# Kernel optimization log

Hardware: AMD Instinct MI355X
Metric: run time of the kernel (lower is better)

Reference implementation:

```python
import jax, jax.numpy as jnp
import numpy as np

B, C, H, W = 4, 320, 32, 32
HEADS = 8
LTXT, DCROSS = 77, 768
HW = H * W


def _ln(x, w, b, eps=1e-5):
    mu = x.mean(-1, keepdims=True)
    var = jnp.var(x, axis=-1, keepdims=True)
    return (x - mu) * jax.lax.rsqrt(var + eps) * w + b


def _gn(x, w, b, groups=32, eps=1e-6):
    Bx, Cx, Hx, Wx = x.shape
    xg = x.reshape(Bx, groups, -1)
    mu = xg.mean(-1, keepdims=True)
    var = jnp.var(xg, axis=-1, keepdims=True)
    xn = ((xg - mu) * jax.lax.rsqrt(var + eps)).reshape(Bx, Cx, Hx, Wx)
    return xn * w[None, :, None, None] + b[None, :, None, None]


def _attn(q, k, v, bias=None):
    Bq, S, Cd = q.shape
    dh = Cd // HEADS
    qh = q.reshape(Bq, S, HEADS, dh)
    kh = k.reshape(Bq, -1, HEADS, dh)
    vh = v.reshape(Bq, -1, HEADS, dh)
    s = jnp.einsum('bqhd,bkhd->bhqk', qh, kh) * (1.0 / np.sqrt(dh))
    if bias is not None:
        s = s + bias  # additive 0/1 otsu mask, exactly as the torch code passes it
    p = jax.nn.softmax(s, axis=-1)
    o = jnp.einsum('bhqk,bkhd->bqhd', p, vh).reshape(Bq, S, Cd)
    return o, p


def _block(x, ctx, prm, bias=None):
    # BasicTransformerBlock: self-attn -> cross-attn (returns probs) -> GEGLU FF
    (ln1w, ln1b, qkv, ow, ob, ln2w, ln2b, q2, kv2, o2w, o2b,
     ln3w, ln3b, ff1w, ff1b, ff2w, ff2b) = prm
    h = _ln(x, ln1w, ln1b)
    q, k, v = jnp.split(h @ qkv, 3, axis=-1)
    o, _ = _attn(q, k, v)
    x = x + o @ ow + ob
    h = _ln(x, ln2w, ln2b)
    k2, v2 = jnp.split(ctx @ kv2, 2, axis=-1)
    o2, p2 = _attn(h @ q2, k2, v2, bias)
    x = x + o2 @ o2w + o2b
    h = _ln(x, ln3w, ln3b)
    a, g = jnp.split(h @ ff1w + ff1b, 2, axis=-1)
    x = x + (a * jax.nn.gelu(g)) @ ff2w + ff2b
    return x, p2


def _otsu(m):
    # vectorized version of the 10-threshold otsu loop (m: [B/2, N])
    mn = m.min(-1, keepdims=True)
    mx = m.max(-1, keepdims=True)
    x = (m - mn) / (mx - mn)
    n = x.shape[-1]
    ts = jnp.arange(10, dtype=x.dtype) * 0.1  # thresholds t*0.1
    low = x[:, None, :] < ts[None, :, None]   # [B/2, 10, N]
    cnt_low = low.sum(-1).astype(x.dtype)
    cnt_high = n - cnt_low
    sum_low = jnp.where(low, x[:, None, :], 0.0).sum(-1)
    sum_high = x.sum(-1, keepdims=True) - sum_low
    mu_low = jnp.where(cnt_low > 0, sum_low / jnp.maximum(cnt_low, 1.0), jnp.nan)
    mu_high = jnp.where(cnt_high > 0, sum_high / jnp.maximum(cnt_high, 1.0), jnp.nan)
    g = (cnt_low / n) * (cnt_high / n) * (mu_low - mu_high) ** 2
    g = jnp.where(jnp.isnan(g), -jnp.inf, g)  # torch: nan > max_g is False -> skipped
    best = jnp.argmax(g, axis=-1)             # first max == torch strict-> ties keep earliest
    gmax = jnp.take_along_axis(g, best[:, None], axis=-1)[:, 0]
    thr = jnp.where(gmax > 0, best.astype(x.dtype) * 0.1, 0.0)[:, None]
    return jnp.where(x < thr, 0.0, jnp.where(x > thr, 1.0, x))


def _fwd(gn_w, gn_b, pin_w, pin_b,
         b_ln1w, b_ln1b, b_qkv, b_ow, b_ob, b_ln2w, b_ln2b, b_q2, b_kv2, b_o2w, b_o2b,
         b_ln3w, b_ln3b, b_ff1w, b_ff1b, b_ff2w, b_ff2b,
         i_ln1w, i_ln1b, i_qkv, i_ow, i_ob, i_ln2w, i_ln2b, i_q2, i_kv2, i_o2w, i_o2b,
         i_ln3w, i_ln3b, i_ff1w, i_ff1b, i_ff2w, i_ff2b,
         pout_w, pout_b, hidden_states, encoder_hidden_states,
         ph_b, ph_t, eot_b, eot_t):
    residual = hidden_states
    h = _gn(hidden_states, gn_w, gn_b)
    h = h.transpose(0, 2, 3, 1).reshape(B, HW, C)
    h = h @ pin_w + pin_b  # use_linear_projection path
    blk = (b_ln1w, b_ln1b, b_qkv, b_ow, b_ob, b_ln2w, b_ln2b, b_q2, b_kv2, b_o2w, b_o2b,
           b_ln3w, b_ln3b, b_ff1w, b_ff1b, b_ff2w, b_ff2b)
    iblk = (i_ln1w, i_ln1b, i_qkv, i_ow, i_ob, i_ln2w, i_ln2b, i_q2, i_kv2, i_o2w, i_o2b,
            i_ln3w, i_ln3b, i_ff1w, i_ff1b, i_ff2w, i_ff2b)
    h, probs = _block(h, encoder_hidden_states, blk)   # probs [B, heads, HW, 77]
    ap = probs.mean(1)[B // 2:]                        # head-avg attn_probs, cond half
    attn = ap.transpose(0, 2, 1)                       # [B/2, 77, HW]
    attn_ph = attn[ph_b, ph_t]                         # [B/2, HW]
    attn_eot = jax.lax.stop_gradient(attn[eot_b, eot_t])
    loss_reg = jnp.mean((attn_ph / attn_ph.max(-1, keepdims=True)
                         - attn_eot / attn_eot.max(-1, keepdims=True)) ** 2)
    mask = _otsu(jax.lax.stop_gradient(attn_ph))       # [B/2, HW]
    bias = mask[:, None, None, :]                      # broadcast over heads and queries
    hs, img = h[:B // 2], h[B // 2:]
    hs, _ = _block(hs, img, iblk, bias)                # image_cross_attention
    h = jnp.concatenate([hs, img], axis=0)
    h = h @ pout_w + pout_b
    sample = h.reshape(B, H, W, C).transpose(0, 3, 1, 2) + residual
    return sample, loss_reg


def setup_inputs():
    key = jax.random.key(0)
    ki = iter(jax.random.split(key, 80))
    f32 = jnp.float32

    def rn(shape, s=0.02):
        return jax.random.normal(next(ki), shape, f32) * s

    def blk(p, cross):
        return {p + 'ln1w': jnp.ones((C,), f32), p + 'ln1b': jnp.zeros((C,), f32),
                p + 'qkv': rn((C, 3 * C)), p + 'ow': rn((C, C)), p + 'ob': jnp.zeros((C,), f32),
                p + 'ln2w': jnp.ones((C,), f32), p + 'ln2b': jnp.zeros((C,), f32),
                p + 'q2': rn((C, C)), p + 'kv2': rn((cross, 2 * C)),
                p + 'o2w': rn((C, C)), p + 'o2b': jnp.zeros((C,), f32),
                p + 'ln3w': jnp.ones((C,), f32), p + 'ln3b': jnp.zeros((C,), f32),
                p + 'ff1w': rn((C, 8 * C)), p + 'ff1b': jnp.zeros((8 * C,), f32),
                p + 'ff2w': rn((4 * C, C)), p + 'ff2b': jnp.zeros((C,), f32)}

    inp = {'gn_w': jnp.ones((C,), f32), 'gn_b': jnp.zeros((C,), f32),
           'pin_w': rn((C, C)), 'pin_b': jnp.zeros((C,), f32)}
    inp.update(blk('b_', DCROSS))
    inp.update(blk('i_', C))
    inp['pout_w'] = rn((C, C))
    inp['pout_b'] = jnp.zeros((C,), f32)
    inp['hidden_states'] = jax.random.normal(next(ki), (B, C, H, W), f32)
    inp['encoder_hidden_states'] = jax.random.normal(next(ki), (B, LTXT, DCROSS), f32)
    inp['ph_b'] = jnp.arange(B // 2)
    inp['ph_t'] = jax.random.randint(next(ki), (B // 2,), 0, LTXT)
    inp['eot_b'] = jnp.arange(B // 2)
    inp['eot_t'] = jax.random.randint(next(ki), (B // 2,), 0, LTXT)
    return inp


def reference(gn_w, gn_b, pin_w, pin_b,
              b_ln1w, b_ln1b, b_qkv, b_ow, b_ob, b_ln2w, b_ln2b, b_q2, b_kv2, b_o2w, b_o2b,
              b_ln3w, b_ln3b, b_ff1w, b_ff1b, b_ff2w, b_ff2b,
              i_ln1w, i_ln1b, i_qkv, i_ow, i_ob, i_ln2w, i_ln2b, i_q2, i_kv2, i_o2w, i_o2b,
              i_ln3w, i_ln3b, i_ff1w, i_ff1b, i_ff2w, i_ff2b,
              pout_w, pout_b, hidden_states, encoder_hidden_states,
              ph_b, ph_t, eot_b, eot_t):
    return _fwd(gn_w, gn_b, pin_w, pin_b,
                b_ln1w, b_ln1b, b_qkv, b_ow, b_ob, b_ln2w, b_ln2b, b_q2, b_kv2, b_o2w, b_o2b,
                b_ln3w, b_ln3b, b_ff1w, b_ff1b, b_ff2w, b_ff2b,
                i_ln1w, i_ln1b, i_qkv, i_ow, i_ob, i_ln2w, i_ln2b, i_q2, i_kv2, i_o2w, i_o2b,
                i_ln3w, i_ln3b, i_ff1w, i_ff1b, i_ff2w, i_ff2b,
                pout_w, pout_b, hidden_states, encoder_hidden_states,
                ph_b, ph_t, eot_b, eot_t)
```

## Files before the change

### kernel.cpp

```cpp
#include <hip/hip_runtime.h>
#include <hip/hip_bf16.h>
#include <math.h>

#define NH 8
#define DH 40
#define CCH 320
#define SCALE 0.15811388300841897f

typedef __attribute__((ext_vector_type(8))) short short8;
typedef __attribute__((ext_vector_type(4))) float float4v;

static __device__ __forceinline__ unsigned short f2bf(float x) {
  __hip_bfloat16 t = __float2bfloat16(x);
  return *reinterpret_cast<unsigned short*>(&t);
}

static __device__ __forceinline__ void gload16(const void* g, void* l) {
  __builtin_amdgcn_global_load_lds((__attribute__((address_space(1))) void*)g,
                                   (__attribute__((address_space(3))) void*)l, 16, 0, 0);
}

__global__ __launch_bounds__(256) void gn_kernel(const float* __restrict__ x,
                                                 const float* __restrict__ w,
                                                 const float* __restrict__ b,
                                                 unsigned short* __restrict__ out) {
  int batch = blockIdx.x >> 5;
  int g = blockIdx.x & 31;
  const int CPG = 10;
  const float* xp = x + ((size_t)batch * CCH + g * CPG) * 1024;
  float s = 0.f, ss = 0.f;
  for (int i = threadIdx.x; i < CPG * 1024; i += 256) { float v = xp[i]; s += v; ss += v * v; }
  __shared__ float r1[256], r2[256];
  r1[threadIdx.x] = s; r2[threadIdx.x] = ss; __syncthreads();
  for (int off = 128; off > 0; off >>= 1) {
    if (threadIdx.x < off) { r1[threadIdx.x] += r1[threadIdx.x + off]; r2[threadIdx.x] += r2[threadIdx.x + off]; }
    __syncthreads();
  }
  float mu = r1[0] * (1.f / 10240.f);
  float var = r2[0] * (1.f / 10240.f) - mu * mu;
  float inv = rsqrtf(var + 1e-6f);
  for (int i = threadIdx.x; i < CPG * 1024; i += 256) {
    int ci = i >> 10; int hw = i & 1023; int c = g * CPG + ci;
    float v = (xp[i] - mu) * inv * w[c] + b[c];
    out[((size_t)batch * 1024 + hw) * CCH + c] = f2bf(v);
  }
}

struct WTab {
  const float* src[16];
  unsigned short* dst[16];
  int Kd[16];
  int Nd[16];
  int perm[16];
  int tstart[17];
  float* lz;
};
__global__ __launch_bounds__(256) void wconv_kernel(WTab t) {
  __shared__ float tile[32][33];
  if (blockIdx.x == 0 && threadIdx.x == 0) *t.lz = 0.f;
  int gid = blockIdx.x;
  int w = 0;
  while (w < 15 && gid >= t.tstart[w + 1]) w++;
  int local = gid - t.tstart[w];
  int K = t.Kd[w], N = t.Nd[w];
  int ntx = (N + 31) >> 5;
  int bx = local % ntx, by = local / ntx;
  int nb = bx * 32, kb = by * 32;
  const float* src = t.src[w];
  unsigned short* dst = t.dst[w];
  int doperm = t.perm[w];
  int half = N >> 1;
  int tx = threadIdx.x & 31, ty = threadIdx.x >> 5;
  for (int i = ty; i < 32; i += 8) {
    int k = kb + i, n = nb + tx;
    tile[i][tx] = (k < K && n < N) ? src[(size_t)k * N + n] : 0.f;
  }
  __syncthreads();
  for (int i = ty; i < 32; i += 8) {
    int n = nb + i, k = kb + tx;
    if (n < N && k < K) {
      int nd = n;
      if (doperm) {
        if (n < half) nd = (n >> 5) * 64 + (n & 31);
        else { int c = n - half; nd = (c >> 5) * 64 + 32 + (c & 31); }
      }
      dst[(size_t)nd * K + k] = f2bf(tile[tx][i]);
    }
  }
}

__global__ __launch_bounds__(256) void lngemm64_kernel(const float* __restrict__ A,
                                                       const float* __restrict__ lnw,
                                                       const float* __restrict__ lnb,
                                                       const unsigned short* __restrict__ Bt,
                                                       const float* __restrict__ bias,
                                                       unsigned short* __restrict__ outp,
                                                       int M, int N, int gl) {
  __shared__ unsigned short As[64][328];
  __shared__ unsigned short Bsd[2][64][32];
  __shared__ float Wf[320], Bf[320];
  __shared__ float Mu[64], Iv[64];
  const int K = 320;
  int tid = threadIdx.x;
  int lane = tid & 63;
  int wv = tid >> 6;
  int quad = lane >> 4;
  int col = lane & 15;
  int m0 = blockIdx.y * 64;
  int n0 = blockIdx.x * 64;
  const unsigned short* bp0 = Bt + (size_t)(n0 + (tid >> 2)) * K + (tid & 3) * 8;
  gload16(bp0, ((char*)Bsd[0]) + wv * 1024);
  for (int i = tid; i < 320; i += 256) { Wf[i] = lnw[i]; Bf[i] = lnb[i]; }
  int l32 = tid & 31;
  int rsub = tid >> 5;
  for (int it = 0; it < 8; it++) {
    int r = it * 8 + rsub;
    const float* ap = A + (size_t)(m0 + r) * K;
    float s = 0.f, ss = 0.f;
#pragma unroll
    for (int j = 0; j < 10; j++) { float v = ap[l32 + j * 32]; s += v; ss += v * v; }
#pragma unroll
    for (int o = 16; o > 0; o >>= 1) { s += __shfl_xor(s, o); ss += __shfl_xor(ss, o); }
    if (l32 == 0) {
      float mu = s * (1.f / 320.f);
      Mu[r] = mu;
      Iv[r] = rsqrtf(ss * (1.f / 320.f) - mu * mu + 1e-5f);
    }
  }
  __syncthreads();
#pragma unroll 4
  for (int i = 0; i < 20; i++) {
    int cc = i * 256 + tid;
    int r = cc / 80, c4 = cc - r * 80;
    int c = c4 * 4;
    float4 v = *(const float4*)(A + (size_t)(m0 + r) * K + c);
    float mu = Mu[r], iv = Iv[r];
    ushort4 o;
    o.x = f2bf((v.x - mu) * iv * Wf[c] + Bf[c]);
    o.y = f2bf((v.y - mu) * iv * Wf[c + 1] + Bf[c + 1]);
    o.z = f2bf((v.z - mu) * iv * Wf[c + 2] + Bf[c + 2]);
    o.w = f2bf((v.w - mu) * iv * Wf[c + 3] + Bf[c + 3]);
    *(ushort4*)&As[r][c] = o;
  }
  __syncthreads();
  float4v acc[4];
  float4v zero = {0.f, 0.f, 0.f, 0.f};
#pragma unroll
  for (int j = 0; j < 4; j++) acc[j] = zero;
  for (int t = 0; t < 10; t++) {
    if (t < 9) gload16(bp0 + (t + 1) * 32, ((char*)Bsd[(t + 1) & 1]) + wv * 1024);
    int k0 = t * 32;
    short8 af = *(short8*)&As[wv * 16 + col][k0 + quad * 8];
#pragma unroll
    for (int j = 0; j < 4; j++) {
      short8 bfr = *(short8*)&Bsd[t & 1][j * 16 + col][quad * 8];
      acc[j] = __builtin_amdgcn_mfma_f32_16x16x32_bf16(af, bfr, acc[j], 0, 0, 0);
    }
    __syncthreads();
  }
  if (gl) {
    int half = N >> 1;
#pragma unroll
    for (int jb = 0; jb < 2; jb++) {
      int nout = (n0 >> 1) + jb * 16 + col;
      float ba = bias[nout];
      float bg = bias[half + nout];
#pragma unroll
      for (int r = 0; r < 4; r++) {
        int m = m0 + wv * 16 + quad * 4 + r;
        float a = acc[jb][r] + ba;
        float g = acc[jb + 2][r] + bg;
        float t2 = tanhf(0.7978845608028654f * (g + 0.044715f * g * g * g));
        outp[(size_t)m * half + nout] = f2bf(a * (0.5f * g * (1.f + t2)));
      }
    }
    return;
  }
#pragma unroll
  for (int j = 0; j < 4; j++) {
    int n = n0 + j * 16 + col;
#pragma unroll
    for (int r = 0; r < 4; r++) {
      int m = m0 + wv * 16 + quad * 4 + r;
      outp[(size_t)m * N + n] = f2bf(acc[j][r]);
    }
  }
}

__global__ __launch_bounds__(256) void mergegemm64_kernel(const float* __restrict__ Opart,
                                                          const float* __restrict__ mpart,
                                                          const float* __restrict__ lpart,
                                                          const unsigned short* __restrict__ Bt,
                                                          const float* __restrict__ bias,
                                                          float* __restrict__ h, int M) {
  __shared__ unsigned short As[64][328];
  __shared__ unsigned short Bsd[2][64][32];
  const int K = 320;
  int tid = threadIdx.x;
  int lane = tid & 63;
  int wv = tid >> 6;
  int quad = lane >> 4;
  int col = lane & 15;
  int m0 = blockIdx.y * 64;
  int n0 = blockIdx.x * 64;
  const unsigned short* bp0 = Bt + (size_t)(n0 + (tid >> 2)) * K + (tid & 3) * 8;
  gload16(bp0, ((char*)Bsd[0]) + wv * 1024);
#pragma unroll
  for (int i = 0; i < 10; i++) {
    int cc = i * 256 + tid;
    int r = cc / 40, c8 = cc - r * 40;
    int c = c8 * 8;
    int hh = c / 40;
    int d = c - hh * 40;
    int m = m0 + r, b = m >> 10, q = m & 1023;
    size_t ri = ((size_t)(b * NH + hh) * 1024 + q) * 4;
    float ma = mpart[ri], mb = mpart[ri + 1], mc = mpart[ri + 2], md = mpart[ri + 3];
    float Mx = fmaxf(fmaxf(ma, mb), fmaxf(mc, md));
    float w0 = __expf(ma - Mx), w1 = __expf(mb - Mx), w2 = __expf(mc - Mx), w3 = __expf(md - Mx);
    float L = lpart[ri] * w0 + lpart[ri + 1] * w1 + lpart[ri + 2] * w2 + lpart[ri + 3] * w3;
    float inv = 1.f / L;
    w0 *= inv; w1 *= inv; w2 *= inv; w3 *= inv;
    const float* p0 = Opart + (ri + 0) * DH + d;
    const float* p1 = Opart + (ri + 1) * DH + d;
    const float* p2 = Opart + (ri + 2) * DH + d;
    const float* p3 = Opart + (ri + 3) * DH + d;
    float4 a0 = *(const float4*)p0, a1 = *(const float4*)p1, a2 = *(const float4*)p2, a3 = *(const float4*)p3;
    float4 b0 = *(const float4*)(p0 + 4), b1 = *(const float4*)(p1 + 4), b2 = *(const float4*)(p2 + 4), b3 = *(const float4*)(p3 + 4);
    ushort4 u0, u1;
    u0.x = f2bf(a0.x * w0 + a1.x * w1 + a2.x * w2 + a3.x * w3);
    u0.y = f2bf(a0.y * w0 + a1.y * w1 + a2.y * w2 + a3.y * w3);
    u0.z = f2bf(a0.z * w0 + a1.z * w1 + a2.z * w2 + a3.z * w3);
    u0.w = f2bf(a0.w * w0 + a1.w * w1 + a2.w * w2 + a3.w * w3);
    u1.x = f2bf(b0.x * w0 + b1.x * w1 + b2.x * w2 + b3.x * w3);
    u1.y = f2bf(b0.y * w0 + b1.y * w1 + b2.y * w2 + b3.y * w3);
    u1.z = f2bf(b0.z * w0 + b1.z * w1 + b2.z * w2 + b3.z * w3);
    u1.w = f2bf(b0.w * w0 + b1.w * w1 + b2.w * w2 + b3.w * w3);
    *(ushort4*)&As[r][c] = u0;
    *(ushort4*)&As[r][c + 4] = u1;
  }
  __syncthreads();
  float4v acc[4];
  float4v zero = {0.f, 0.f, 0.f, 0.f};
#pragma unroll
  for (int j = 0; j < 4; j++) acc[j] = zero;
  for (int t = 0; t < 10; t++) {
    if (t < 9) gload16(bp0 + (t + 1) * 32, ((char*)Bsd[(t + 1) & 1]) + wv * 1024);
    int k0 = t * 32;
    short8 af = *(short8*)&As[wv * 16 + col][k0 + quad * 8];
#pragma unroll
    for (int j = 0; j < 4; j++) {
      short8 bfr = *(short8*)&Bsd[t & 1][j * 16 + col][quad * 8];
      acc[j] = __builtin_amdgcn_mfma_f32_16x16x32_bf16(af, bfr, acc[j], 0, 0, 0);
    }
    __syncthreads();
  }
#pragma unroll
  for (int j = 0; j < 4; j++) {
    int n = n0 + j * 16 + col;
    float bv = bias[n];
#pragma unroll
    for (int r = 0; r < 4; r++) {
      int m = m0 + wv * 16 + quad * 4 + r;
      size_t oi = (size_t)m * 320 + n;
      h[oi] = acc[j][r] + bv + h[oi];
    }
  }
}

__global__ __launch_bounds__(256) void mgemm64_kernel(const void* __restrict__ Ap,
                                                      const unsigned short* __restrict__ Bt,
                                                      const float* __restrict__ bias,
                                                      const float* __restrict__ res,
                                                      void* __restrict__ outp,
                                                      int M, int N, int K, int a32, int omode) {
  __shared__ unsigned short As[64][160];
  __shared__ unsigned short Bs[64][160];
  int tid = threadIdx.x;
  int lane = tid & 63;
  int wv = tid >> 6;
  int quad = lane >> 4;
  int col = lane & 15;
  int m0 = blockIdx.y * 64;
  int n0 = blockIdx.x * 64;
  float4v acc[4];
  float4v zero = {0.f, 0.f, 0.f, 0.f};
#pragma unroll
  for (int j = 0; j < 4; j++) acc[j] = zero;
  short8 vzero = {0, 0, 0, 0, 0, 0, 0, 0};
  int kfast = (!a32) && ((K % 160) == 0);
  int off[5];
#pragma unroll
  for (int i = 0; i < 5; i++) { int c = i * 256 + tid; int row = c / 20; off[i] = row * K + (c - row * 20) * 8; }
  int wb = (tid & 192) * 16;
  const unsigned short* Ab = (const unsigned short*)Ap + (size_t)m0 * K;
  const unsigned short* Bb = Bt + (size_t)n0 * K;
  for (int k0 = 0; k0 < K; k0 += 160) {
    if (kfast) {
#pragma unroll
      for (int i = 0; i < 5; i++) {
        gload16(Ab + off[i] + k0, ((char*)As) + wb + i * 4096);
        gload16(Bb + off[i] + k0, ((char*)Bs) + wb + i * 4096);
      }
    } else {
#pragma unroll
      for (int i = 0; i < 5; i++) {
        int u = tid + i * 256;
        int row = u / 20, seg = u - row * 20;
        int k = k0 + seg * 8;
        int m = m0 + row;
        short8 av = vzero;
        if (m < M && k < K) {
          if (a32) {
            const float* Af = (const float*)Ap;
            float4 f0 = *(const float4*)(Af + (size_t)m * K + k);
            float4 f1 = *(const float4*)(Af + (size_t)m * K + k + 4);
            av[0] = (short)f2bf(f0.x); av[1] = (short)f2bf(f0.y);
            av[2] = (short)f2bf(f0.z); av[3] = (short)f2bf(f0.w);
            av[4] = (short)f2bf(f1.x); av[5] = (short)f2bf(f1.y);
            av[6] = (short)f2bf(f1.z); av[7] = (short)f2bf(f1.w);
          } else {
            av = *(const short8*)((const unsigned short*)Ap + (size_t)m * K + k);
          }
        }
        *(short8*)&As[row][seg * 8] = av;
        int n = n0 + row;
        short8 bv = vzero;
        if (n < N && k < K) bv = *(const short8*)(Bt + (size_t)n * K + k);
        *(short8*)&Bs[row][seg * 8] = bv;
      }
    }
    __syncthreads();
#pragma unroll
    for (int kk = 0; kk < 5; kk++) {
      int kq2 = kk * 32 + quad * 8;
      short8 af = *(short8*)&As[wv * 16 + col][kq2];
#pragma unroll
      for (int j = 0; j < 4; j++) {
        short8 bfr = *(short8*)&Bs[j * 16 + col][kq2];
        acc[j] = __builtin_amdgcn_mfma_f32_16x16x32_bf16(af, bfr, acc[j], 0, 0, 0);
      }
    }
    __syncthreads();
  }
#pragma unroll
  for (int j = 0; j < 4; j++) {
    int n = n0 + j * 16 + col;
    if (n >= N) continue;
    float bv = bias ? bias[n] : 0.f;
#pragma unroll
    for (int r = 0; r < 4; r++) {
      int m = m0 + wv * 16 + quad * 4 + r;
      if (m < M) {
        float v = acc[j][r] + bv;
        if (omode == 2) {
          int bq = m >> 10, hw = m & 1023;
          size_t oi = ((size_t)bq * N + n) * 1024 + hw;
          ((float*)outp)[oi] = v + res[oi];
        } else {
          if (res) v += res[(size_t)m * N + n];
          if (omode == 1) ((unsigned short*)outp)[(size_t)m * N + n] = f2bf(v);
          else ((float*)outp)[(size_t)m * N + n] = v;
        }
      }
    }
  }
}

#define VSTR 72
__global__ __launch_bounds__(256) void mfattns_kernel(const unsigned short* __restrict__ qp, int qstr,
                                                      const unsigned short* __restrict__ kp, int kstr,
                                                      const unsigned short* __restrict__ vp, int vstr,
                                                      const float* __restrict__ bias,
                                                      float* __restrict__ Opart,
                                                      float* __restrict__ mpart,
                                                      float* __restrict__ lpart) {
  __shared__ unsigned short Ks[64 * 56];
  __shared__ unsigned short Vt[48 * VSTR];
  __shared__ unsigned short Ps[4][16 * 72];
  int tid = threadIdx.x;
  int lane = tid & 63;
  int wv = tid >> 6;
  int quad = lane >> 4;
  int col = lane & 15;
  int bid = blockIdx.x;
  int split = bid & 3;
  int qt = (bid >> 2) & 15;
  int h = (bid >> 6) & 7;
  int b = bid >> 9;

  short8 zero8 = {0, 0, 0, 0, 0, 0, 0, 0};
  int qrow = qt * 64 + wv * 16 + col;
  const unsigned short* qbase = qp + (size_t)(b * 1024 + qrow) * qstr + h * DH;
  short8 qf0 = *(const short8*)(qbase + quad * 8);
  short8 qf1 = (quad == 0) ? *(const short8*)(qbase + 32) : zero8;

  float4v Oacc[3];
  float4v fzero = {0.f, 0.f, 0.f, 0.f};
  Oacc[0] = fzero; Oacc[1] = fzero; Oacc[2] = fzero;
  float mr[4] = {-3.4e38f, -3.4e38f, -3.4e38f, -3.4e38f};
  float lr[4] = {0.f, 0.f, 0.f, 0.f};

  for (int kt = split * 4; kt < split * 4 + 4; kt++) {
    int kb = kt * 64;
    __syncthreads();
    for (int u = tid; u < 384; u += 256) {
      int key = u / 6, s = u - key * 6;
      short8 kv8 = zero8;
      if (s < 5) kv8 = *(const short8*)(kp + (size_t)(b * 1024 + kb + key) * kstr + h * DH + s * 8);
      *(short8*)&Ks[key * 56 + s * 8] = kv8;
    }
    for (int u = tid; u < 384; u += 256) {
      int s = u >> 6, key = u & 63;
      short8 vv8 = zero8;
      if (s < 5) vv8 = *(const short8*)(vp + (size_t)(b * 1024 + kb + key) * vstr + h * DH + s * 8);
#pragma unroll
      for (int j = 0; j < 8; j++) Vt[(s * 8 + j) * VSTR + key] = (unsigned short)vv8[j];
    }
    __syncthreads();

    float4v sf[4];
#pragma unroll
    for (int jb = 0; jb < 4; jb++) {
      const unsigned short* krow = &Ks[(jb * 16 + col) * 56];
      short8 bk0 = *(const short8*)(krow + quad * 8);
      short8 bk1 = (quad == 0) ? *(const short8*)(krow + 32) : zero8;
      float4v s = fzero;
      s = __builtin_amdgcn_mfma_f32_16x16x32_bf16(qf0, bk0, s, 0, 0, 0);
      s = __builtin_amdgcn_mfma_f32_16x16x32_bf16(qf1, bk1, s, 0, 0, 0);
      float bv = bias ? bias[b * 1024 + kb + jb * 16 + col] : 0.f;
#pragma unroll
      for (int r = 0; r < 4; r++) s[r] = s[r] * SCALE + bv;
      sf[jb] = s;
    }
    float tmax[4];
#pragma unroll
    for (int r = 0; r < 4; r++) {
      float t = fmaxf(fmaxf(sf[0][r], sf[1][r]), fmaxf(sf[2][r], sf[3][r]));
#pragma unroll
      for (int o = 1; o < 16; o <<= 1) t = fmaxf(t, __shfl_xor(t, o));
      tmax[r] = t;
    }
    float al[4];
#pragma unroll
    for (int r = 0; r < 4; r++) {
      float mnew = fmaxf(mr[r], tmax[r]);
      al[r] = __expf(mr[r] - mnew);
      mr[r] = mnew;
      lr[r] *= al[r];
    }
#pragma unroll
    for (int nb = 0; nb < 3; nb++)
#pragma unroll
      for (int r = 0; r < 4; r++) Oacc[nb][r] *= al[r];
    float rs[4] = {0.f, 0.f, 0.f, 0.f};
#pragma unroll
    for (int jb = 0; jb < 4; jb++) {
#pragma unroll
      for (int r = 0; r < 4; r++) {
        float p = __expf(sf[jb][r] - mr[r]);
        rs[r] += p;
        Ps[wv][(quad * 4 + r) * 72 + jb * 16 + col] = f2bf(p);
      }
    }
#pragma unroll
    for (int r = 0; r < 4; r++) {
      float t = rs[r];
#pragma unroll
      for (int o = 1; o < 16; o <<= 1) t += __shfl_xor(t, o);
      lr[r] += t;
    }
#pragma unroll
    for (int kc = 0; kc < 2; kc++) {
      int koff = kc * 32 + quad * 8;
      short8 pa = *(const short8*)&Ps[wv][col * 72 + koff];
#pragma unroll
      for (int nb = 0; nb < 3; nb++) {
        short8 vb = *(const short8*)&Vt[(nb * 16 + col) * VSTR + koff];
        Oacc[nb] = __builtin_amdgcn_mfma_f32_16x16x32_bf16(pa, vb, Oacc[nb], 0, 0, 0);
      }
    }
  }
#pragma unroll
  for (int r = 0; r < 4; r++) {
    int qo = qt * 64 + wv * 16 + quad * 4 + r;
    size_t rowidx = (size_t)(b * NH + h) * 1024 + qo;
    float* orow = Opart + (rowidx * 4 + split) * DH;
#pragma unroll
    for (int nb = 0; nb < 3; nb++) {
      int d = nb * 16 + col;
      if (d < DH) orow[d] = Oacc[nb][r];
    }
    if (col == 0) {
      mpart[rowidx * 4 + split] = mr[r];
      lpart[rowidx * 4 + split] = lr[r];
    }
  }
}

#define CVSTR 104
__global__ __launch_bounds__(256) void cattnm_kernel(const unsigned short* __restrict__ qp,
                                                     const unsigned short* __restrict__ kvp,
                                                     unsigned short* __restrict__ op,
                                                     float* __restrict__ probs) {
  __shared__ unsigned short Ks[80 * 56];
  __shared__ unsigned short Vt[48 * CVSTR];
  __shared__ unsigned short Ps[4][16 * 104];
  int tid = threadIdx.x;
  int lane = tid & 63;
  int wv = tid >> 6;
  int quad = lane >> 4;
  int col = lane & 15;
  int bid = blockIdx.x;
  int qt = bid & 15;
  int h = (bid >> 4) & 7;
  int b = bid >> 7;

  short8 zero8 = {0, 0, 0, 0, 0, 0, 0, 0};
  for (int u = tid; u < 480; u += 256) {
    int key = u / 6, s = u - key * 6;
    short8 v8 = zero8;
    if (s < 5 && key < 77) v8 = *(const short8*)(kvp + (size_t)(b * 77 + key) * 640 + h * DH + s * 8);
    *(short8*)&Ks[key * 56 + s * 8] = v8;
  }
  for (int u = tid; u < 576; u += 256) {
    int s = u / 96, key = u - s * 96;
    short8 v8 = zero8;
    if (s < 5 && key < 77) v8 = *(const short8*)(kvp + (size_t)(b * 77 + key) * 640 + 320 + h * DH + s * 8);
#pragma unroll
    for (int j = 0; j < 8; j++) Vt[(s * 8 + j) * CVSTR + key] = (unsigned short)v8[j];
  }
  int qrow = qt * 64 + wv * 16 + col;
  const unsigned short* qbase = qp + (size_t)(b * 1024 + qrow) * CCH + h * DH;
  short8 qf0 = *(const short8*)(qbase + quad * 8);
  short8 qf1 = (quad == 0) ? *(const short8*)(qbase + 32) : zero8;
  __syncthreads();

  float4v fzero = {0.f, 0.f, 0.f, 0.f};
  float4v sf[5];
#pragma unroll
  for (int jb = 0; jb < 5; jb++) {
    const unsigned short* krow = &Ks[(jb * 16 + col) * 56];
    short8 bk0 = *(const short8*)(krow + quad * 8);
    short8 bk1 = (quad == 0) ? *(const short8*)(krow + 32) : zero8;
    float4v s = fzero;
    s = __builtin_amdgcn_mfma_f32_16x16x32_bf16(qf0, bk0, s, 0, 0, 0);
    s = __builtin_amdgcn_mfma_f32_16x16x32_bf16(qf1, bk1, s, 0, 0, 0);
    int key = jb * 16 + col;
    float msk = (key < 77) ? 0.f : -3.4e38f;
#pragma unroll
    for (int r = 0; r < 4; r++) s[r] = s[r] * SCALE + msk;
    sf[jb] = s;
  }
  float inv[4];
#pragma unroll
  for (int r = 0; r < 4; r++) {
    float t = sf[0][r];
#pragma unroll
    for (int jb = 1; jb < 5; jb++) t = fmaxf(t, sf[jb][r]);
#pragma unroll
    for (int o = 1; o < 16; o <<= 1) t = fmaxf(t, __shfl_xor(t, o));
    float sum = 0.f;
#pragma unroll
    for (int jb = 0; jb < 5; jb++) { float e = __expf(sf[jb][r] - t); sf[jb][r] = e; sum += e; }
#pragma unroll
    for (int o = 1; o < 16; o <<= 1) sum += __shfl_xor(sum, o);
    inv[r] = 1.f / sum;
  }
#pragma unroll
  for (int jb = 0; jb < 5; jb++) {
    int key = jb * 16 + col;
    float4v pv;
#pragma unroll
    for (int r = 0; r < 4; r++) {
      float p = sf[jb][r] * inv[r];
      Ps[wv][(quad * 4 + r) * 104 + jb * 16 + col] = f2bf(p);
      pv[r] = p;
    }
    if (b >= 2 && key < 77) {
      size_t pi = ((size_t)((b - 2) * NH + h) * 77 + key) * 1024 + qt * 64 + wv * 16 + quad * 4;
      *(float4v*)&probs[pi] = pv;
    }
  }
  float4v Oacc[3];
  Oacc[0] = fzero; Oacc[1] = fzero; Oacc[2] = fzero;
#pragma unroll
  for (int kc = 0; kc < 3; kc++) {
    int koff = kc * 32 + quad * 8;
    short8 pa = (koff < 80) ? *(const short8*)&Ps[wv][col * 104 + koff] : zero8;
#pragma unroll
    for (int nb = 0; nb < 3; nb++) {
      short8 vb = *(const short8*)&Vt[(nb * 16 + col) * CVSTR + koff];
      Oacc[nb] = __builtin_amdgcn_mfma_f32_16x16x32_bf16(pa, vb, Oacc[nb], 0, 0, 0);
    }
  }
#pragma unroll
  for (int r = 0; r < 4; r++) {
    int qo = qt * 64 + wv * 16 + quad * 4 + r;
    unsigned short* orow = op + (size_t)(b * 1024 + qo) * CCH + h * DH;
#pragma unroll
    for (int nb = 0; nb < 3; nb++) {
      int d = nb * 16 + col;
      if (d < DH) orow[d] = f2bf(Oacc[nb][r]);
    }
  }
}

__global__ __launch_bounds__(256) void eol_kernel(const float* __restrict__ pT,
                                                  const int* __restrict__ phb, const int* __restrict__ pht,
                                                  const int* __restrict__ eob, const int* __restrict__ eot,
                                                  float* __restrict__ mask,
                                                  float* __restrict__ lossout) {
  __shared__ float S[4][24];
  __shared__ float shthr;
  int i = blockIdx.x, tid = threadIdx.x;
  int lane = tid & 63, wv = tid >> 6;
  int pb = phb[i], pt = pht[i], eb = eob[i], et = eot[i];
  float x[4], y[4];
#pragma unroll
  for (int j = 0; j < 4; j++) {
    int q = tid + 256 * j;
    float s1 = 0.f, s2 = 0.f;
#pragma unroll
    for (int hh = 0; hh < NH; hh++) {
      s1 += pT[((size_t)(pb * NH + hh) * 77 + pt) * 1024 + q];
      s2 += pT[((size_t)(eb * NH + hh) * 77 + et) * 1024 + q];
    }
    x[j] = s1 * 0.125f;
    y[j] = s2 * 0.125f;
  }
  float mx = fmaxf(fmaxf(x[0], x[1]), fmaxf(x[2], x[3]));
  float me = fmaxf(fmaxf(y[0], y[1]), fmaxf(y[2], y[3]));
  float mn = fminf(fminf(x[0], x[1]), fminf(x[2], x[3]));
  float sx = x[0] + x[1] + x[2] + x[3];
#pragma unroll
  for (int o = 32; o > 0; o >>= 1) {
    mx = fmaxf(mx, __shfl_xor(mx, o));
    me = fmaxf(me, __shfl_xor(me, o));
    mn = fminf(mn, __shfl_xor(mn, o));
    sx += __shfl_xor(sx, o);
  }
  if (lane == 0) { S[wv][0] = mx; S[wv][1] = me; S[wv][2] = mn; S[wv][3] = sx; }
  __syncthreads();
  mx = fmaxf(fmaxf(S[0][0], S[1][0]), fmaxf(S[2][0], S[3][0]));
  me = fmaxf(fmaxf(S[0][1], S[1][1]), fmaxf(S[2][1], S[3][1]));
  mn = fminf(fminf(S[0][2], S[1][2]), fminf(S[2][2], S[3][2]));
  sx = S[0][3] + S[1][3] + S[2][3] + S[3][3];
  float invmp = 1.f / mx, invme = 1.f / me;
  float inv = 1.f / (mx - mn);
  float lp = 0.f;
  float cnt[10], sm[10];
#pragma unroll
  for (int t = 0; t < 10; t++) { cnt[t] = 0.f; sm[t] = 0.f; }
#pragma unroll
  for (int j = 0; j < 4; j++) {
    float d = x[j] * invmp - y[j] * invme;
    lp += d * d;
    float v = (x[j] - mn) * inv;
#pragma unroll
    for (int t = 0; t < 10; t++) {
      if (v < t * 0.1f) { cnt[t] += 1.f; sm[t] += v; }
    }
  }
#pragma unroll
  for (int o = 32; o > 0; o >>= 1) {
    lp += __shfl_xor(lp, o);
#pragma unroll
    for (int t = 0; t < 10; t++) { cnt[t] += __shfl_xor(cnt[t], o); sm[t] += __shfl_xor(sm[t], o); }
  }
  __syncthreads();
  if (lane == 0) {
    S[wv][0] = lp;
#pragma unroll
    for (int t = 0; t < 10; t++) { S[wv][1 + t] = cnt[t]; S[wv][11 + t] = sm[t]; }
  }
  __syncthreads();
  if (tid == 0) {
    float lpt = S[0][0] + S[1][0] + S[2][0] + S[3][0];
    atomicAdd(lossout, lpt * (1.f / 2048.f));
    float total = (sx - 1024.f * mn) * inv;
    float gmax = -3.4e38f; int best = 0;
    for (int t = 0; t < 10; t++) {
      float c_low = S[0][1 + t] + S[1][1 + t] + S[2][1 + t] + S[3][1 + t];
      float s_low = S[0][11 + t] + S[1][11 + t] + S[2][11 + t] + S[3][11 + t];
      float c_high = 1024.f - c_low;
      float g;
      if (c_low > 0.f && c_high > 0.f) {
        float mu_l = s_low / c_low;
        float mu_h = (total - s_low) / c_high;
        float dd = mu_l - mu_h;
        g = (c_low * (1.f / 1024.f)) * (c_high * (1.f / 1024.f)) * dd * dd;
      } else g = -3.4e38f;
      if (g > gmax) { gmax = g; best = t; }
    }
    shthr = (gmax > 0.f) ? best * 0.1f : 0.f;
  }
  __syncthreads();
  float thr = shthr;
#pragma unroll
  for (int j = 0; j < 4; j++) {
    int q = tid + 256 * j;
    float v = (x[j] - mn) * inv;
    mask[i * 1024 + q] = (v < thr) ? 0.f : ((v > thr) ? 1.f : v);
  }
}

extern "C" void kernel_launch(void* const* d_in, const int* in_sizes, int n_in,
                              void* d_out, int out_size, void* d_ws, size_t ws_size,
                              hipStream_t stream) {
  auto F = [&](int i) { return (const float*)d_in[i]; };
  auto I = [&](int i) { return (const int*)d_in[i]; };

  float* ws = (float*)d_ws;
  float* h    = ws;
  float* ffb  = h    + 1310720;
  float* p2   = ffb  + 10485760;
  float* mask = p2   + 2523136;

  float* Opart = ffb;
  float* mpart = ffb + 5242880;
  float* lpart = ffb + 5242880 + 131072;

  unsigned short* b16   = (unsigned short*)(mask + 2048);
  unsigned short* lnb16 = b16;
  unsigned short* attb16= lnb16 + 1310720;
  unsigned short* actb16= attb16 + 1310720;
  unsigned short* qkv16 = actb16 + 5242880;
  unsigned short* q16   = qkv16 + 3932160;
  unsigned short* kv16  = q16 + 1310720;
  unsigned short* wptr  = kv16 + 1310720;

  auto walloc = [&](int n) { unsigned short* p = wptr; wptr += n; return p; };
  unsigned short* pin_t  = walloc(102400);
  unsigned short* bqkv_t = walloc(307200);
  unsigned short* bow_t  = walloc(102400);
  unsigned short* bq2_t  = walloc(102400);
  unsigned short* bkv2_t = walloc(491520);
  unsigned short* bo2_t  = walloc(102400);
  unsigned short* bff1_t = walloc(819200);
  unsigned short* bff2_t = walloc(409600);
  unsigned short* iqkv_t = walloc(307200);
  unsigned short* iow_t  = walloc(102400);
  unsigned short* iq2_t  = walloc(102400);
  unsigned short* ikv2_t = walloc(204800);
  unsigned short* io2_t  = walloc(102400);
  unsigned short* iff1_t = walloc(819200);
  unsigned short* iff2_t = walloc(409600);
  unsigned short* pout_t = walloc(102400);

  float* out = (float*)d_out;

  WTab wt;
  wt.lz = out + 1310720;
  int nt = 0, cnt = 0;
  auto addw = [&](const float* s, unsigned short* d, int K, int N, int perm) {
    wt.src[cnt] = s; wt.dst[cnt] = d; wt.Kd[cnt] = K; wt.Nd[cnt] = N; wt.perm[cnt] = perm;
    wt.tstart[cnt] = nt;
    nt += ((K + 31) / 32) * ((N + 31) / 32);
    cnt++;
  };
  addw(F(2), pin_t, 320, 320, 0);
  addw(F(4 + 2), bqkv_t, 320, 960, 0);
  addw(F(4 + 3), bow_t, 320, 320, 0);
  addw(F(4 + 7), bq2_t, 320, 320, 0);
  addw(F(4 + 8), bkv2_t, 768, 640, 0);
  addw(F(4 + 9), bo2_t, 320, 320, 0);
  addw(F(4 + 13), bff1_t, 320, 2560, 1);
  addw(F(4 + 15), bff2_t, 1280, 320, 0);
  addw(F(21 + 2), iqkv_t, 320, 960, 0);
  addw(F(21 + 3), iow_t, 320, 320, 0);
  addw(F(21 + 7), iq2_t, 320, 320, 0);
  addw(F(21 + 8), ikv2_t, 320, 640, 0);
  addw(F(21 + 9), io2_t, 320, 320, 0);
  addw(F(21 + 13), iff1_t, 320, 2560, 1);
  addw(F(21 + 15), iff2_t, 1280, 320, 0);
  addw(F(38), pout_t, 320, 320, 0);
  wt.tstart[16] = nt;

  wconv_kernel<<<nt, 256, 0, stream>>>(wt);

  auto gemm64 = [&](const void* A, const unsigned short* Wt, const float* bias,
                    const float* res, void* o, int M, int N, int K, int a32, int omode) {
    dim3 g((N + 63) / 64, (M + 63) / 64);
    mgemm64_kernel<<<g, 256, 0, stream>>>(A, Wt, bias, res, o, M, N, K, a32, omode);
  };
  auto lngemm = [&](const float* A, const float* lw, const float* lb,
                    const unsigned short* Wt, const float* bias,
                    unsigned short* o, int M, int N, int gl) {
    dim3 g(N / 64, M / 64);
    lngemm64_kernel<<<g, 256, 0, stream>>>(A, lw, lb, Wt, bias, o, M, N, gl);
  };
  auto mergegemm = [&](const unsigned short* Wt, const float* bias, int M) {
    dim3 g(5, M / 64);
    mergegemm64_kernel<<<g, 256, 0, stream>>>(Opart, mpart, lpart, Wt, bias, h, M);
  };

  gn_kernel<<<128, 256, 0, stream>>>(F(40), F(0), F(1), lnb16);
  gemm64(lnb16, pin_t, F(3), nullptr, h, 4096, 320, 320, 0, 0);

  auto run_block = [&](int p, int Bx, bool img_block,
                       const unsigned short* qkv_t, const unsigned short* ow_t,
                       const unsigned short* q2_t, const unsigned short* kv2_t,
                       const unsigned short* o2_t, const unsigned short* ff1_t,
                       const unsigned short* ff2_t) {
    int M = Bx * 1024;
    lngemm(h, F(p + 0), F(p + 1), qkv_t, nullptr, qkv16, M, 960, 0);
    mfattns_kernel<<<Bx * 512, 256, 0, stream>>>(qkv16, 960, qkv16 + 320, 960, qkv16 + 640, 960,
                                                 nullptr, Opart, mpart, lpart);
    mergegemm(ow_t, F(p + 4), M);
    lngemm(h, F(p + 5), F(p + 6), q2_t, nullptr, q16, M, 320, 0);
    if (!img_block) {
      gemm64(F(41), kv2_t, nullptr, nullptr, kv16, Bx * 77, 640, 768, 1, 1);
      cattnm_kernel<<<Bx * 128, 256, 0, stream>>>(q16, kv16, attb16, p2);
      gemm64(attb16, o2_t, F(p + 10), h, h, M, 320, 320, 0, 0);
    } else {
      gemm64(h + (size_t)2 * 1024 * 320, kv2_t, nullptr, nullptr, kv16, Bx * 1024, 640, 320, 1, 1);
      mfattns_kernel<<<Bx * 512, 256, 0, stream>>>(q16, 320, kv16, 640, kv16 + 320, 640,
                                                   mask, Opart, mpart, lpart);
      mergegemm(o2_t, F(p + 10), M);
    }
    lngemm(h, F(p + 11), F(p + 12), ff1_t, F(p + 14), actb16, M, 2560, 1);
    gemm64(actb16, ff2_t, F(p + 16), h, h, M, 320, 1280, 0, 0);
  };

  run_block(4, 4, false, bqkv_t, bow_t, bq2_t, bkv2_t, bo2_t, bff1_t, bff2_t);

  eol_kernel<<<2, 256, 0, stream>>>(p2, I(42), I(43), I(44), I(45), mask, out + 1310720);

  run_block(21, 2, true, iqkv_t, iow_t, iq2_t, ikv2_t, io2_t, iff1_t, iff2_t);

  gemm64(h, pout_t, F(39), F(40), out, 4096, 320, 320, 1, 2);
}
```

Measured before the change: 574.5 us.

## Widen LN-GEMM N tiles and switch LDS tiles to chunk-major layout

```diff
diff --git a/kernel.cpp b/kernel.cpp
--- a/kernel.cpp
+++ b/kernel.cpp
@@ -89,6 +89,7 @@
   }
 }
 
+template <int NT>
 __global__ __launch_bounds__(256) void lngemm64_kernel(const float* __restrict__ A,
                                                        const float* __restrict__ lnw,
                                                        const float* __restrict__ lnb,
@@ -97,7 +98,7 @@
                                                        unsigned short* __restrict__ outp,
                                                        int M, int N, int gl) {
   __shared__ unsigned short As[64][328];
-  __shared__ unsigned short Bsd[2][64][32];
+  __shared__ unsigned short Bsd[2 * NT * 4 * 64 * 8];
   __shared__ float Wf[320], Bf[320];
   __shared__ float Mu[64], Iv[64];
   const int K = 320;
@@ -107,9 +108,13 @@
   int quad = lane >> 4;
   int col = lane & 15;
   int m0 = blockIdx.y * 64;
-  int n0 = blockIdx.x * 64;
-  const unsigned short* bp0 = Bt + (size_t)(n0 + (tid >> 2)) * K + (tid & 3) * 8;
-  gload16(bp0, ((char*)Bsd[0]) + wv * 1024);
+  int n0 = blockIdx.x * 64 * NT;
+  char* bsb = (char*)Bsd;
+  const unsigned short* bp[NT];
+#pragma unroll
+  for (int jj = 0; jj < NT; jj++) bp[jj] = Bt + (size_t)(n0 + jj * 64 + lane) * K + wv * 8;
+#pragma unroll
+  for (int jj = 0; jj < NT; jj++) gload16(bp[jj], bsb + jj * 4096 + wv * 1024);
   for (int i = tid; i < 320; i += 256) { Wf[i] = lnw[i]; Bf[i] = lnb[i]; }
   int l32 = tid & 31;
   int rsub = tid >> 5;
@@ -143,48 +148,63 @@
     *(ushort4*)&As[r][c] = o;
   }
   __syncthreads();
-  float4v acc[4];
+  float4v acc[NT][4];
   float4v zero = {0.f, 0.f, 0.f, 0.f};
 #pragma unroll
-  for (int j = 0; j < 4; j++) acc[j] = zero;
+  for (int jj = 0; jj < NT; jj++)
+#pragma unroll
+    for (int j = 0; j < 4; j++) acc[jj][j] = zero;
   for (int t = 0; t < 10; t++) {
-    if (t < 9) gload16(bp0 + (t + 1) * 32, ((char*)Bsd[(t + 1) & 1]) + wv * 1024);
+    if (t < 9) {
+      char* dst = bsb + ((t + 1) & 1) * NT * 4096;
+#pragma unroll
+      for (int jj = 0; jj < NT; jj++) gload16(bp[jj] + (t + 1) * 32, dst + jj * 4096 + wv * 1024);
+    }
     int k0 = t * 32;
     short8 af = *(short8*)&As[wv * 16 + col][k0 + quad * 8];
-#pragma unroll
-    for (int j = 0; j < 4; j++) {
-      short8 bfr = *(short8*)&Bsd[t & 1][j * 16 + col][quad * 8];
-      acc[j] = __builtin_amdgcn_mfma_f32_16x16x32_bf16(af, bfr, acc[j], 0, 0, 0);
-    }
+    const char* rb = bsb + (t & 1) * NT * 4096 + quad * 1024 + col * 16;
+#pragma unroll
+    for (int jj = 0; jj < NT; jj++)
+#pragma unroll
+      for (int j = 0; j < 4; j++) {
+        short8 bfr = *(const short8*)(rb + jj * 4096 + j * 256);
+        acc[jj][j] = __builtin_amdgcn_mfma_f32_16x16x32_bf16(af, bfr, acc[jj][j], 0, 0, 0);
+      }
     __syncthreads();
   }
   if (gl) {
     int half = N >> 1;
 #pragma unroll
-    for (int jb = 0; jb < 2; jb++) {
-      int nout = (n0 >> 1) + jb * 16 + col;
-      float ba = bias[nout];
-      float bg = bias[half + nout];
+    for (int jj = 0; jj < NT; jj++) {
+      int nbase = (n0 + jj * 64) >> 1;
+#pragma unroll
+      for (int jb = 0; jb < 2; jb++) {
+        int nout = nbase + jb * 16 + col;
+        float ba = bias[nout];
+        float bg = bias[half + nout];
+#pragma unroll
+        for (int r = 0; r < 4; r++) {
+          int m = m0 + wv * 16 + quad * 4 + r;
+          float a = acc[jj][jb][r] + ba;
+          float g = acc[jj][jb + 2][r] + bg;
+          float t2 = tanhf(0.7978845608028654f * (g + 0.044715f * g * g * g));
+          outp[(size_t)m * half + nout] = f2bf(a * (0.5f * g * (1.f + t2)));
+        }
+      }
+    }
+    return;
+  }
+#pragma unroll
+  for (int jj = 0; jj < NT; jj++)
+#pragma unroll
+    for (int j = 0; j < 4; j++) {
+      int n = n0 + jj * 64 + j * 16 + col;
 #pragma unroll
       for (int r = 0; r < 4; r++) {
         int m = m0 + wv * 16 + quad * 4 + r;
-        float a = acc[jb][r] + ba;
-        float g = acc[jb + 2][r] + bg;
-        float t2 = tanhf(0.7978845608028654f * (g + 0.044715f * g * g * g));
-        outp[(size_t)m * half + nout] = f2bf(a * (0.5f * g * (1.f + t2)));
-      }
-    }
-    return;
-  }
-#pragma unroll
-  for (int j = 0; j < 4; j++) {
-    int n = n0 + j * 16 + col;
-#pragma unroll
-    for (int r = 0; r < 4; r++) {
-      int m = m0 + wv * 16 + quad * 4 + r;
-      outp[(size_t)m * N + n] = f2bf(acc[j][r]);
-    }
-  }
+        outp[(size_t)m * N + n] = f2bf(acc[jj][j][r]);
+      }
+    }
 }
 
 __global__ __launch_bounds__(256) void mergegemm64_kernel(const float* __restrict__ Opart,
@@ -194,7 +214,7 @@
                                                           const float* __restrict__ bias,
                                                           float* __restrict__ h, int M) {
   __shared__ unsigned short As[64][328];
-  __shared__ unsigned short Bsd[2][64][32];
+  __shared__ unsigned short Bsd[2 * 4 * 64 * 8];
   const int K = 320;
   int tid = threadIdx.x;
   int lane = tid & 63;
@@ -203,8 +223,9 @@
   int col = lane & 15;
   int m0 = blockIdx.y * 64;
   int n0 = blockIdx.x * 64;
-  const unsigned short* bp0 = Bt + (size_t)(n0 + (tid >> 2)) * K + (tid & 3) * 8;
-  gload16(bp0, ((char*)Bsd[0]) + wv * 1024);
+  char* bsb = (char*)Bsd;
+  const unsigned short* bp0 = Bt + (size_t)(n0 + lane) * K + wv * 8;
+  gload16(bp0, bsb + wv * 1024);
 #pragma unroll
   for (int i = 0; i < 10; i++) {
     int cc = i * 256 + tid;
@@ -244,12 +265,13 @@
 #pragma unroll
   for (int j = 0; j < 4; j++) acc[j] = zero;
   for (int t = 0; t < 10; t++) {
-    if (t < 9) gload16(bp0 + (t + 1) * 32, ((char*)Bsd[(t + 1) & 1]) + wv * 1024);
+    if (t < 9) gload16(bp0 + (t + 1) * 32, bsb + ((t + 1) & 1) * 4096 + wv * 1024);
     int k0 = t * 32;
     short8 af = *(short8*)&As[wv * 16 + col][k0 + quad * 8];
+    const char* rb = bsb + (t & 1) * 4096 + quad * 1024 + col * 16;
 #pragma unroll
     for (int j = 0; j < 4; j++) {
-      short8 bfr = *(short8*)&Bsd[t & 1][j * 16 + col][quad * 8];
+      short8 bfr = *(const short8*)(rb + j * 256);
       acc[j] = __builtin_amdgcn_mfma_f32_16x16x32_bf16(af, bfr, acc[j], 0, 0, 0);
     }
     __syncthreads();
@@ -273,8 +295,8 @@
                                                       const float* __restrict__ res,
                                                       void* __restrict__ outp,
                                                       int M, int N, int K, int a32, int omode) {
-  __shared__ unsigned short As[64][160];
-  __shared__ unsigned short Bs[64][160];
+  __shared__ unsigned short As[5 * 4 * 64 * 8];
+  __shared__ unsigned short Bs[5 * 4 * 64 * 8];
   int tid = threadIdx.x;
   int lane = tid & 63;
   int wv = tid >> 6;
@@ -282,32 +304,29 @@
   int col = lane & 15;
   int m0 = blockIdx.y * 64;
   int n0 = blockIdx.x * 64;
+  char* asb = (char*)As;
+  char* bsb = (char*)Bs;
   float4v acc[4];
   float4v zero = {0.f, 0.f, 0.f, 0.f};
 #pragma unroll
   for (int j = 0; j < 4; j++) acc[j] = zero;
   short8 vzero = {0, 0, 0, 0, 0, 0, 0, 0};
   int kfast = (!a32) && ((K % 160) == 0);
-  int off[5];
-#pragma unroll
-  for (int i = 0; i < 5; i++) { int c = i * 256 + tid; int row = c / 20; off[i] = row * K + (c - row * 20) * 8; }
-  int wb = (tid & 192) * 16;
-  const unsigned short* Ab = (const unsigned short*)Ap + (size_t)m0 * K;
-  const unsigned short* Bb = Bt + (size_t)n0 * K;
+  const unsigned short* Ab = (const unsigned short*)Ap + (size_t)(m0 + lane) * K + wv * 8;
+  const unsigned short* Bb = Bt + (size_t)(n0 + lane) * K + wv * 8;
   for (int k0 = 0; k0 < K; k0 += 160) {
     if (kfast) {
 #pragma unroll
       for (int i = 0; i < 5; i++) {
-        gload16(Ab + off[i] + k0, ((char*)As) + wb + i * 4096);
-        gload16(Bb + off[i] + k0, ((char*)Bs) + wb + i * 4096);
+        gload16(Ab + k0 + i * 32, asb + i * 4096 + wv * 1024);
+        gload16(Bb + k0 + i * 32, bsb + i * 4096 + wv * 1024);
       }
     } else {
+      int m = m0 + lane;
+      int n = n0 + lane;
 #pragma unroll
       for (int i = 0; i < 5; i++) {
-        int u = tid + i * 256;
-        int row = u / 20, seg = u - row * 20;
-        int k = k0 + seg * 8;
-        int m = m0 + row;
+        int k = k0 + i * 32 + wv * 8;
         short8 av = vzero;
         if (m < M && k < K) {
           if (a32) {
@@ -322,21 +341,19 @@
             av = *(const short8*)((const unsigned short*)Ap + (size_t)m * K + k);
           }
         }
-        *(short8*)&As[row][seg * 8] = av;
-        int n = n0 + row;
+        *(short8*)(asb + i * 4096 + wv * 1024 + lane * 16) = av;
         short8 bv = vzero;
         if (n < N && k < K) bv = *(const short8*)(Bt + (size_t)n * K + k);
-        *(short8*)&Bs[row][seg * 8] = bv;
+        *(short8*)(bsb + i * 4096 + wv * 1024 + lane * 16) = bv;
       }
     }
     __syncthreads();
 #pragma unroll
     for (int kk = 0; kk < 5; kk++) {
-      int kq2 = kk * 32 + quad * 8;
-      short8 af = *(short8*)&As[wv * 16 + col][kq2];
+      short8 af = *(const short8*)(asb + kk * 4096 + quad * 1024 + (wv * 16 + col) * 16);
 #pragma unroll
       for (int j = 0; j < 4; j++) {
-        short8 bfr = *(short8*)&Bs[j * 16 + col][kq2];
+        short8 bfr = *(const short8*)(bsb + kk * 4096 + quad * 1024 + (j * 16 + col) * 16);
         acc[j] = __builtin_amdgcn_mfma_f32_16x16x32_bf16(af, bfr, acc[j], 0, 0, 0);
       }
     }
@@ -785,9 +802,17 @@
   };
   auto lngemm = [&](const float* A, const float* lw, const float* lb,
                     const unsigned short* Wt, const float* bias,
-                    unsigned short* o, int M, int N, int gl) {
-    dim3 g(N / 64, M / 64);
-    lngemm64_kernel<<<g, 256, 0, stream>>>(A, lw, lb, Wt, bias, o, M, N, gl);
+                    unsigned short* o, int M, int N, int NT, int gl) {
+    if (NT == 4) {
+      dim3 g(N / 256, M / 64);
+      lngemm64_kernel<4><<<g, 256, 0, stream>>>(A, lw, lb, Wt, bias, o, M, N, gl);
+    } else if (NT == 3) {
+      dim3 g(N / 192, M / 64);
+      lngemm64_kernel<3><<<g, 256, 0, stream>>>(A, lw, lb, Wt, bias, o, M, N, gl);
+    } else {
+      dim3 g(N / 64, M / 64);
+      lngemm64_kernel<1><<<g, 256, 0, stream>>>(A, lw, lb, Wt, bias, o, M, N, gl);
+    }
   };
   auto mergegemm = [&](const unsigned short* Wt, const float* bias, int M) {
     dim3 g(5, M / 64);
@@ -803,11 +828,11 @@
                        const unsigned short* o2_t, const unsigned short* ff1_t,
                        const unsigned short* ff2_t) {
     int M = Bx * 1024;
-    lngemm(h, F(p + 0), F(p + 1), qkv_t, nullptr, qkv16, M, 960, 0);
+    lngemm(h, F(p + 0), F(p + 1), qkv_t, nullptr, qkv16, M, 960, 3, 0);
     mfattns_kernel<<<Bx * 512, 256, 0, stream>>>(qkv16, 960, qkv16 + 320, 960, qkv16 + 640, 960,
                                                  nullptr, Opart, mpart, lpart);
     mergegemm(ow_t, F(p + 4), M);
-    lngemm(h, F(p + 5), F(p + 6), q2_t, nullptr, q16, M, 320, 0);
+    lngemm(h, F(p + 5), F(p + 6), q2_t, nullptr, q16, M, 320, 1, 0);
     if (!img_block) {
       gemm64(F(41), kv2_t, nullptr, nullptr, kv16, Bx * 77, 640, 768, 1, 1);
       cattnm_kernel<<<Bx * 128, 256, 0, stream>>>(q16, kv16, attb16, p2);
@@ -818,7 +843,7 @@
                                                    mask, Opart, mpart, lpart);
       mergegemm(o2_t, F(p + 10), M);
     }
-    lngemm(h, F(p + 11), F(p + 12), ff1_t, F(p + 14), actb16, M, 2560, 1);
+    lngemm(h, F(p + 11), F(p + 12), ff1_t, F(p + 14), actb16, M, 2560, 4, 1);
     gemm64(actb16, ff2_t, F(p + 16), h, h, M, 320, 1280, 0, 0);
   };
 
```

Result: slower. 643.3 us (+12.0%).
